# Kernel optimization log

Hardware: AMD Instinct MI355X
Metric: run time of the kernel (lower is better)

## Reference

```python
import jax, jax.numpy as jnp
import numpy as np

B, N, D, H = 2, 4096, 256, 8
HD = D // H
NEG_SLOPE = 0.01
LN_EPS = 1e-5


def setup_inputs() -> dict:
    key = jax.random.key(0)
    ks = jax.random.split(key, 6)
    s = 1.0 / np.sqrt(D)
    return {
        "h": jax.random.normal(ks[0], (B, N, D), dtype=jnp.float32),
        "W_l": jax.random.normal(ks[1], (D, D), dtype=jnp.float32) * s,
        "W_r": jax.random.normal(ks[2], (D, D), dtype=jnp.float32) * s,
        "a_l": jax.random.normal(ks[3], (HD,), dtype=jnp.float32) * s,
        "a_r": jax.random.normal(ks[4], (HD,), dtype=jnp.float32) * s,
        "W_final": jax.random.normal(ks[5], (D, D), dtype=jnp.float32) * s,
        "ln_g": jnp.ones((D,), dtype=jnp.float32),
        "ln_b": jnp.zeros((D,), dtype=jnp.float32),
    }


def _leaky(x):
    return jnp.where(x >= 0, x, NEG_SLOPE * x)


def reference(h, W_l, W_r, a_l, a_r, W_final, ln_g, ln_b):
    b, n, d = h.shape
    # projections -> [b, H, n, HD]
    fl = (h @ W_l).reshape(b, n, H, HD).transpose(0, 2, 1, 3)
    fr = (h @ W_r).reshape(b, n, H, HD).transpose(0, 2, 1, 3)
    # additive GAT-style scores: [b, H, n] each, broadcast to [b, H, n, n]
    sl = jnp.einsum("bhnd,d->bhn", _leaky(fl), a_l)
    sr = jnp.einsum("bhnd,d->bhn", _leaky(fr), a_r)
    score = sl[..., :, None] + sr[..., None, :]  # [b, H, n, n]
    attn = jnp.mean(score, axis=1)  # pre-softmax mean over heads: [b, n, n]
    p = jax.nn.softmax(score, axis=-1)  # dropout is identity (eval / p=0)
    context = jnp.einsum("bhij,bhjd->bhid", p, fr)  # [b, H, n, HD]
    h_sa = context.transpose(0, 2, 1, 3).reshape(b, n, d)
    fh = h_sa @ W_final
    x = h + fh
    mu = jnp.mean(x, axis=-1, keepdims=True)
    var = jnp.mean(jnp.square(x - mu), axis=-1, keepdims=True)
    h_out = (x - mu) * jax.lax.rsqrt(var + LN_EPS) * ln_g + ln_b
    return (h_out, attn)
```

## Files before the change

kernel.cpp:

```cpp
#include <hip/hip_runtime.h>
#include <hip/hip_bf16.h>

#define BATCH 2
#define SEQ   4096
#define DIM   256
#define HEADS 8
#define HDIM  32
#define M_ROWS (BATCH * SEQ)
#define JCHUNK 32
#define NCHUNK (SEQ / JCHUNK)

typedef short bf16x8 __attribute__((ext_vector_type(8)));
typedef unsigned short u16x8 __attribute__((ext_vector_type(8)));
typedef float f32x4 __attribute__((ext_vector_type(4)));

static __device__ inline unsigned short f2bf(float x) {
  union { float f; unsigned u; } v; v.f = x;
  unsigned r = v.u + 0x7FFF + ((v.u >> 16) & 1);
  return (unsigned short)(r >> 16);
}

__global__ __launch_bounds__(256) void k_prep(const float* __restrict__ Wl,
                                              const float* __restrict__ Wr,
                                              unsigned short* __restrict__ Wt) {
  __shared__ float tile[32][33];
  const int k0 = blockIdx.x * 32;
  const int n0 = blockIdx.y * 32;
  const int t = threadIdx.x;
  const float* W = (n0 < 256) ? Wl : Wr;
  const int nb = n0 & 255;
  {
    const int r = t >> 3;
    const int c = (t & 7) * 4;
    const float4 v = *(const float4*)(&W[(size_t)(k0 + r) * DIM + nb + c]);
    tile[r][c + 0] = v.x; tile[r][c + 1] = v.y;
    tile[r][c + 2] = v.z; tile[r][c + 3] = v.w;
  }
  __syncthreads();
  {
    const int nl = t >> 3;
    const int kl = (t & 7) * 4;
    ushort4 o;
    o.x = f2bf(tile[kl + 0][nl]); o.y = f2bf(tile[kl + 1][nl]);
    o.z = f2bf(tile[kl + 2][nl]); o.w = f2bf(tile[kl + 3][nl]);
    *(ushort4*)(&Wt[(size_t)(n0 + nl) * DIM + k0 + kl]) = o;
  }
}

__global__ __launch_bounds__(512) void k_gemm_fused(
    const float* __restrict__ A, const unsigned short* __restrict__ Wt,
    const float* __restrict__ a_l, const float* __restrict__ a_r,
    float* __restrict__ fr, float* __restrict__ sr,
    float* __restrict__ msl, float* __restrict__ msr) {
  __shared__ unsigned short As[64 * 32];
  __shared__ unsigned short Bs[256 * 32];
  __shared__ float red[64][8];

  const int bid = blockIdx.x;
  const int isR = bid & 1;
  const int bm  = bid >> 1;
  const int m0 = bm * 64;
  const int n0 = isR * 256;

  const int t = threadIdx.x;
  const int lane = t & 63;
  const int wid = t >> 6;

  f32x4 acc[4][2];
  #pragma unroll
  for (int i = 0; i < 4; ++i)
    #pragma unroll
    for (int j = 0; j < 2; ++j) acc[i][j] = (f32x4){0.f, 0.f, 0.f, 0.f};

  for (int k0 = 0; k0 < DIM; k0 += 32) {
    if (t < 256) {
      const int row = t >> 2;
      const int kc = t & 3;
      const int slot = kc ^ ((row >> 1) & 3);
      const float4 a0 = *(const float4*)(&A[(size_t)(m0 + row) * DIM + k0 + kc * 8]);
      const float4 a1 = *(const float4*)(&A[(size_t)(m0 + row) * DIM + k0 + kc * 8 + 4]);
      u16x8 pa;
      pa[0] = f2bf(a0.x); pa[1] = f2bf(a0.y); pa[2] = f2bf(a0.z); pa[3] = f2bf(a0.w);
      pa[4] = f2bf(a1.x); pa[5] = f2bf(a1.y); pa[6] = f2bf(a1.z); pa[7] = f2bf(a1.w);
      *(u16x8*)((char*)As + row * 64 + slot * 16) = pa;
    }
    #pragma unroll
    for (int p = 0; p < 2; ++p) {
      const int task = t + p * 512;
      const int row = task >> 2;
      const int kc = task & 3;
      const int slot = kc ^ ((row >> 1) & 3);
      const u16x8 pb = *(const u16x8*)(&Wt[(size_t)(n0 + row) * DIM + k0 + kc * 8]);
      *(u16x8*)((char*)Bs + row * 64 + slot * 16) = pb;
    }
    __syncthreads();

    bf16x8 af[4], bfr[2];
    #pragma unroll
    for (int mr = 0; mr < 4; ++mr) {
      const int ra = mr * 16 + (lane & 15);
      const int sl = (lane >> 4) ^ ((ra >> 1) & 3);
      af[mr] = *(const bf16x8*)((const char*)As + ra * 64 + sl * 16);
    }
    #pragma unroll
    for (int nr = 0; nr < 2; ++nr) {
      const int cb = wid * 32 + nr * 16 + (lane & 15);
      const int sl = (lane >> 4) ^ ((cb >> 1) & 3);
      bfr[nr] = *(const bf16x8*)((const char*)Bs + cb * 64 + sl * 16);
    }
    #pragma unroll
    for (int mr = 0; mr < 4; ++mr)
      #pragma unroll
      for (int nr = 0; nr < 2; ++nr)
        acc[mr][nr] = __builtin_amdgcn_mfma_f32_16x16x32_bf16(af[mr], bfr[nr], acc[mr][nr], 0, 0, 0);
    __syncthreads();
  }

  const float* av = isR ? a_r : a_l;
  const int b = m0 >> 12;
  const int nbase = m0 & 4095;

  #pragma unroll
  for (int mr = 0; mr < 4; ++mr) {
    #pragma unroll
    for (int r = 0; r < 4; ++r) {
      float p = 0.f;
      #pragma unroll
      for (int nr = 0; nr < 2; ++nr) {
        float x = acc[mr][nr][r];
        x = x >= 0.f ? x : 0.01f * x;
        p = fmaf(x, av[nr * 16 + (lane & 15)], p);
      }
      #pragma unroll
      for (int o = 1; o < 16; o <<= 1) p += __shfl_xor(p, o, 16);
      if ((lane & 15) == 0) {
        const int rl = mr * 16 + (lane >> 4) * 4 + r;
        red[rl][wid] = p;
        if (isR) sr[((size_t)(b * HEADS + wid)) * SEQ + nbase + rl] = p;
      }
    }
  }
  __syncthreads();
  if (t < 64) {
    float s = 0.f;
    #pragma unroll
    for (int h2 = 0; h2 < 8; ++h2) s += red[t][h2];
    (isR ? msr : msl)[m0 + t] = s * 0.125f;
  }
  if (isR) {
    #pragma unroll
    for (int mr = 0; mr < 4; ++mr)
      #pragma unroll
      for (int nr = 0; nr < 2; ++nr) {
        const int col = wid * 32 + nr * 16 + (lane & 15);
        #pragma unroll
        for (int r = 0; r < 4; ++r) {
          const int row = m0 + mr * 16 + (lane >> 4) * 4 + r;
          fr[(size_t)row * DIM + col] = acc[mr][nr][r];
        }
      }
  }
}

__global__ __launch_bounds__(256) void k_ctx(const float* __restrict__ sr,
                                             const float* __restrict__ fr,
                                             float* __restrict__ cpart,
                                             float* __restrict__ wpart) {
  const int b  = blockIdx.x >> 7;
  const int jc = blockIdx.x & 127;
  const int j0 = jc * JCHUNK;
  const int t = threadIdx.x;
  __shared__ float ws_[HEADS][JCHUNK];

  {
    const int h2 = t >> 5, jj = t & 31;
    float e = expf(sr[((size_t)(b * HEADS + h2)) * SEQ + j0 + jj]);
    ws_[h2][jj] = e;
    float s = e;
    #pragma unroll
    for (int o = 16; o > 0; o >>= 1) s += __shfl_xor(s, o, 32);
    if (jj == 0) wpart[(size_t)(b * NCHUNK + jc) * HEADS + h2] = s;
  }
  __syncthreads();

  const int h2 = t >> 5;
  const float* frb = fr + (size_t)(b * SEQ + j0) * DIM + t;
  float accv = 0.f;
  #pragma unroll 8
  for (int jj = 0; jj < JCHUNK; ++jj)
    accv = fmaf(ws_[h2][jj], frb[(size_t)jj * DIM], accv);
  cpart[(size_t)(b * NCHUNK + jc) * DIM + t] = accv;
}

__global__ __launch_bounds__(256) void k_fh(const float* __restrict__ cpart,
                                            const float* __restrict__ wpart,
                                            const float* __restrict__ Wf,
                                            float* __restrict__ fhp) {
  const int b = blockIdx.x >> 3;
  const int kc = blockIdx.x & 7;
  const int t = threadIdx.x;
  __shared__ float credu[8][32];
  __shared__ float c_s[32];
  __shared__ float wred[128];

  {
    const int jg = t >> 5, kl = t & 31;
    float p = 0.f;
    #pragma unroll
    for (int jc = jg; jc < NCHUNK; jc += 8)
      p += cpart[(size_t)(b * NCHUNK + jc) * DIM + kc * HDIM + kl];
    credu[jg][kl] = p;
  }
  if (t < 128) wred[t] = wpart[(size_t)(b * NCHUNK + t) * HEADS + kc];
  __syncthreads();
  if (t < 32) {
    float s = 0.f;
    #pragma unroll
    for (int g2 = 0; g2 < 8; ++g2) s += credu[g2][t];
    float wsum = 0.f;
    #pragma unroll
    for (int i = 0; i < 128; ++i) wsum += wred[i];
    c_s[t] = s / wsum;
  }
  __syncthreads();

  float a2 = 0.f;
  #pragma unroll 8
  for (int kl = 0; kl < HDIM; ++kl)
    a2 = fmaf(c_s[kl], Wf[(size_t)(kc * HDIM + kl) * DIM + t], a2);
  fhp[(size_t)(b * HEADS + kc) * DIM + t] = a2;
}

__global__ __launch_bounds__(256) void k_ln_attn(const float* __restrict__ h,
                                                 const float* __restrict__ fhp,
                                                 const float* __restrict__ g,
                                                 const float* __restrict__ bb,
                                                 const float* __restrict__ msl,
                                                 const float* __restrict__ msr,
                                                 float* __restrict__ out,
                                                 float* __restrict__ attn) {
  const int row = blockIdx.x;
  const int b = row >> 12;
  const int t = threadIdx.x;
  float fh = 0.f;
  #pragma unroll
  for (int h2 = 0; h2 < 8; ++h2) fh += fhp[(size_t)(b * HEADS + h2) * DIM + t];
  const float x = h[(size_t)row * DIM + t] + fh;
  float s1 = x, s2 = x * x;
  #pragma unroll
  for (int o = 32; o > 0; o >>= 1) {
    s1 += __shfl_xor(s1, o, 64);
    s2 += __shfl_xor(s2, o, 64);
  }
  __shared__ float r1[4], r2[4];
  if ((t & 63) == 0) { r1[t >> 6] = s1; r2[t >> 6] = s2; }
  __syncthreads();
  s1 = r1[0] + r1[1] + r1[2] + r1[3];
  s2 = r2[0] + r2[1] + r2[2] + r2[3];
  const float mu = s1 * (1.f / 256.f);
  const float var = s2 * (1.f / 256.f) - mu * mu;
  const float rs = rsqrtf(var + 1e-5f);
  out[(size_t)row * DIM + t] = (x - mu) * rs * g[t] + bb[t];

  const float v = msl[row];
  const f32x4* mr4 = (const f32x4*)(msr + ((size_t)b << 12));
  f32x4* dst = (f32x4*)(attn + ((size_t)row << 12));
  #pragma unroll
  for (int q = 0; q < 4; ++q) {
    f32x4 m4 = mr4[q * 256 + t];
    __builtin_nontemporal_store(m4 + v, &dst[q * 256 + t]);
  }
}

extern "C" void kernel_launch(void* const* d_in, const int* in_sizes, int n_in,
                              void* d_out, int out_size, void* d_ws, size_t ws_size,
                              hipStream_t stream) {
  const float* h  = (const float*)d_in[0];
  const float* Wl = (const float*)d_in[1];
  const float* Wr = (const float*)d_in[2];
  const float* al = (const float*)d_in[3];
  const float* ar = (const float*)d_in[4];
  const float* Wf = (const float*)d_in[5];
  const float* g  = (const float*)d_in[6];
  const float* bb = (const float*)d_in[7];
  float* out = (float*)d_out;
  float* ws  = (float*)d_ws;

  float* fr    = ws;
  float* srs   = fr + (size_t)M_ROWS * DIM;
  float* msl   = srs + BATCH * HEADS * SEQ;
  float* msr   = msl + M_ROWS;
  float* cpart = msr + M_ROWS;
  float* wpart = cpart + BATCH * NCHUNK * DIM;
  float* fhp   = wpart + BATCH * NCHUNK * HEADS;
  unsigned short* Wt = (unsigned short*)(fhp + BATCH * HEADS * DIM);

  k_prep<<<dim3(8, 16), 256, 0, stream>>>(Wl, Wr, Wt);
  k_gemm_fused<<<256, 512, 0, stream>>>(h, Wt, al, ar, fr, srs, msl, msr);
  k_ctx<<<BATCH * NCHUNK, 256, 0, stream>>>(srs, fr, cpart, wpart);
  k_fh<<<BATCH * HEADS, 256, 0, stream>>>(cpart, wpart, Wf, fhp);
  k_ln_attn<<<M_ROWS, 256, 0, stream>>>(h, fhp, g, bb, msl, msr,
                                        out, out + (size_t)M_ROWS * DIM);
}
```

Measured before the change: 56.97 us.

## Merge ctx, fh and attn-store into one kernel with last-block reduction

Combines the context partial kernel, the Wf projection kernel and the large attn broadcast store into one launch. The ctx blocks take a global atomic counter, and the last one to finish reduces the partials and computes fh for both batches. The remaining blocks write the attn matrix at the same time. LayerNorm becomes its own small kernel that reads the finished fh. The aim is to remove launch gaps and to overlap the serial ctx→fh chain with the bandwidth-heavy attn writes. The cost is that a single block does the whole Wf GEMV serially, and correctness now depends on the counter being reset in k_prep on every call.

```diff
diff --git a/kernel.cpp b/kernel.cpp
--- a/kernel.cpp
+++ b/kernel.cpp
@@ -9,6 +9,7 @@
 #define M_ROWS (BATCH * SEQ)
 #define JCHUNK 32
 #define NCHUNK (SEQ / JCHUNK)
+#define CTXBLKS (BATCH * NCHUNK)
 
 typedef short bf16x8 __attribute__((ext_vector_type(8)));
 typedef unsigned short u16x8 __attribute__((ext_vector_type(8)));
@@ -22,7 +23,9 @@
 
 __global__ __launch_bounds__(256) void k_prep(const float* __restrict__ Wl,
                                               const float* __restrict__ Wr,
-                                              unsigned short* __restrict__ Wt) {
+                                              unsigned short* __restrict__ Wt,
+                                              unsigned* __restrict__ ctr) {
+  if (blockIdx.x == 0 && blockIdx.y == 0 && threadIdx.x == 0) *ctr = 0u;
   __shared__ float tile[32][33];
   const int k0 = blockIdx.x * 32;
   const int n0 = blockIdx.y * 32;
@@ -162,90 +165,95 @@
   }
 }
 
-__global__ __launch_bounds__(256) void k_ctx(const float* __restrict__ sr,
-                                             const float* __restrict__ fr,
-                                             float* __restrict__ cpart,
-                                             float* __restrict__ wpart) {
-  const int b  = blockIdx.x >> 7;
-  const int jc = blockIdx.x & 127;
-  const int j0 = jc * JCHUNK;
+__global__ __launch_bounds__(256) void k_mega(const float* __restrict__ sr,
+                                              const float* __restrict__ fr,
+                                              const float* __restrict__ Wf,
+                                              const float* __restrict__ msl,
+                                              const float* __restrict__ msr,
+                                              float* __restrict__ cpart,
+                                              float* __restrict__ wpart,
+                                              float* __restrict__ fh2,
+                                              float* __restrict__ attn,
+                                              unsigned* __restrict__ ctr) {
+  const int blk = blockIdx.x;
   const int t = threadIdx.x;
   __shared__ float ws_[HEADS][JCHUNK];
-
-  {
-    const int h2 = t >> 5, jj = t & 31;
-    float e = expf(sr[((size_t)(b * HEADS + h2)) * SEQ + j0 + jj]);
-    ws_[h2][jj] = e;
-    float s = e;
-    #pragma unroll
-    for (int o = 16; o > 0; o >>= 1) s += __shfl_xor(s, o, 32);
-    if (jj == 0) wpart[(size_t)(b * NCHUNK + jc) * HEADS + h2] = s;
-  }
-  __syncthreads();
-
-  const int h2 = t >> 5;
-  const float* frb = fr + (size_t)(b * SEQ + j0) * DIM + t;
-  float accv = 0.f;
-  #pragma unroll 8
-  for (int jj = 0; jj < JCHUNK; ++jj)
-    accv = fmaf(ws_[h2][jj], frb[(size_t)jj * DIM], accv);
-  cpart[(size_t)(b * NCHUNK + jc) * DIM + t] = accv;
-}
-
-__global__ __launch_bounds__(256) void k_fh(const float* __restrict__ cpart,
-                                            const float* __restrict__ wpart,
-                                            const float* __restrict__ Wf,
-                                            float* __restrict__ fhp) {
-  const int b = blockIdx.x >> 3;
-  const int kc = blockIdx.x & 7;
-  const int t = threadIdx.x;
-  __shared__ float credu[8][32];
-  __shared__ float c_s[32];
-  __shared__ float wred[128];
-
-  {
-    const int jg = t >> 5, kl = t & 31;
-    float p = 0.f;
-    #pragma unroll
-    for (int jc = jg; jc < NCHUNK; jc += 8)
-      p += cpart[(size_t)(b * NCHUNK + jc) * DIM + kc * HDIM + kl];
-    credu[jg][kl] = p;
-  }
-  if (t < 128) wred[t] = wpart[(size_t)(b * NCHUNK + t) * HEADS + kc];
-  __syncthreads();
-  if (t < 32) {
-    float s = 0.f;
-    #pragma unroll
-    for (int g2 = 0; g2 < 8; ++g2) s += credu[g2][t];
-    float wsum = 0.f;
-    #pragma unroll
-    for (int i = 0; i < 128; ++i) wsum += wred[i];
-    c_s[t] = s / wsum;
-  }
-  __syncthreads();
-
-  float a2 = 0.f;
-  #pragma unroll 8
-  for (int kl = 0; kl < HDIM; ++kl)
-    a2 = fmaf(c_s[kl], Wf[(size_t)(kc * HDIM + kl) * DIM + t], a2);
-  fhp[(size_t)(b * HEADS + kc) * DIM + t] = a2;
-}
-
-__global__ __launch_bounds__(256) void k_ln_attn(const float* __restrict__ h,
-                                                 const float* __restrict__ fhp,
-                                                 const float* __restrict__ g,
-                                                 const float* __restrict__ bb,
-                                                 const float* __restrict__ msl,
-                                                 const float* __restrict__ msr,
-                                                 float* __restrict__ out,
-                                                 float* __restrict__ attn) {
+  __shared__ float wred[HEADS];
+  __shared__ float c_s[DIM];
+  __shared__ unsigned done_s;
+
+  if (blk < CTXBLKS) {
+    const int b  = blk >> 7;
+    const int jc = blk & 127;
+    const int j0 = jc * JCHUNK;
+    {
+      const int h2 = t >> 5, jj = t & 31;
+      float e = expf(sr[((size_t)(b * HEADS + h2)) * SEQ + j0 + jj]);
+      ws_[h2][jj] = e;
+      float s = e;
+      #pragma unroll
+      for (int o = 16; o > 0; o >>= 1) s += __shfl_xor(s, o, 32);
+      if (jj == 0) wpart[(size_t)(b * NCHUNK + jc) * HEADS + h2] = s;
+    }
+    __syncthreads();
+    {
+      const int h2 = t >> 5;
+      const float* frb = fr + (size_t)(b * SEQ + j0) * DIM + t;
+      float accv = 0.f;
+      #pragma unroll 8
+      for (int jj = 0; jj < JCHUNK; ++jj)
+        accv = fmaf(ws_[h2][jj], frb[(size_t)jj * DIM], accv);
+      cpart[(size_t)(b * NCHUNK + jc) * DIM + t] = accv;
+    }
+    __threadfence();
+    if (t == 0) done_s = atomicAdd(ctr, 1u);
+    __syncthreads();
+    if (done_s == CTXBLKS - 1) {
+      __threadfence();
+      for (int b2 = 0; b2 < BATCH; ++b2) {
+        if (t < HEADS) {
+          float s = 0.f;
+          for (int jc2 = 0; jc2 < NCHUNK; ++jc2)
+            s += wpart[(size_t)(b2 * NCHUNK + jc2) * HEADS + t];
+          wred[t] = s;
+        }
+        float c = 0.f;
+        for (int jc2 = 0; jc2 < NCHUNK; ++jc2)
+          c += cpart[(size_t)(b2 * NCHUNK + jc2) * DIM + t];
+        __syncthreads();
+        c_s[t] = c / wred[t >> 5];
+        __syncthreads();
+        float a2 = 0.f;
+        #pragma unroll 8
+        for (int k = 0; k < DIM; ++k)
+          a2 = fmaf(c_s[k], Wf[(size_t)k * DIM + t], a2);
+        fh2[b2 * DIM + t] = a2;
+        __syncthreads();
+      }
+    }
+  } else {
+    const int row = blk - CTXBLKS;
+    const int b = row >> 12;
+    const float v = msl[row];
+    const f32x4* mr4 = (const f32x4*)(msr + ((size_t)b << 12));
+    f32x4* dst = (f32x4*)(attn + ((size_t)row << 12));
+    #pragma unroll
+    for (int q = 0; q < 4; ++q) {
+      f32x4 m4 = mr4[q * 256 + t];
+      __builtin_nontemporal_store(m4 + v, &dst[q * 256 + t]);
+    }
+  }
+}
+
+__global__ __launch_bounds__(256) void k_ln(const float* __restrict__ h,
+                                            const float* __restrict__ fh2,
+                                            const float* __restrict__ g,
+                                            const float* __restrict__ bb,
+                                            float* __restrict__ out) {
   const int row = blockIdx.x;
   const int b = row >> 12;
   const int t = threadIdx.x;
-  float fh = 0.f;
-  #pragma unroll
-  for (int h2 = 0; h2 < 8; ++h2) fh += fhp[(size_t)(b * HEADS + h2) * DIM + t];
-  const float x = h[(size_t)row * DIM + t] + fh;
+  const float x = h[(size_t)row * DIM + t] + fh2[b * DIM + t];
   float s1 = x, s2 = x * x;
   #pragma unroll
   for (int o = 32; o > 0; o >>= 1) {
@@ -261,15 +269,6 @@
   const float var = s2 * (1.f / 256.f) - mu * mu;
   const float rs = rsqrtf(var + 1e-5f);
   out[(size_t)row * DIM + t] = (x - mu) * rs * g[t] + bb[t];
-
-  const float v = msl[row];
-  const f32x4* mr4 = (const f32x4*)(msr + ((size_t)b << 12));
-  f32x4* dst = (f32x4*)(attn + ((size_t)row << 12));
-  #pragma unroll
-  for (int q = 0; q < 4; ++q) {
-    f32x4 m4 = mr4[q * 256 + t];
-    __builtin_nontemporal_store(m4 + v, &dst[q * 256 + t]);
-  }
 }
 
 extern "C" void kernel_launch(void* const* d_in, const int* in_sizes, int n_in,
@@ -292,13 +291,14 @@
   float* msr   = msl + M_ROWS;
   float* cpart = msr + M_ROWS;
   float* wpart = cpart + BATCH * NCHUNK * DIM;
-  float* fhp   = wpart + BATCH * NCHUNK * HEADS;
-  unsigned short* Wt = (unsigned short*)(fhp + BATCH * HEADS * DIM);
-
-  k_prep<<<dim3(8, 16), 256, 0, stream>>>(Wl, Wr, Wt);
+  float* fh2   = wpart + BATCH * NCHUNK * HEADS;
+  unsigned short* Wt = (unsigned short*)(fh2 + BATCH * DIM);
+  unsigned* ctr = (unsigned*)(Wt + 512 * DIM);
+
+  k_prep<<<dim3(8, 16), 256, 0, stream>>>(Wl, Wr, Wt, ctr);
   k_gemm_fused<<<256, 512, 0, stream>>>(h, Wt, al, ar, fr, srs, msl, msr);
-  k_ctx<<<BATCH * NCHUNK, 256, 0, stream>>>(srs, fr, cpart, wpart);
-  k_fh<<<BATCH * HEADS, 256, 0, stream>>>(cpart, wpart, Wf, fhp);
-  k_ln_attn<<<M_ROWS, 256, 0, stream>>>(h, fhp, g, bb, msl, msr,
-                                        out, out + (size_t)M_ROWS * DIM);
-}
+  k_mega<<<CTXBLKS + M_ROWS, 256, 0, stream>>>(srs, fr, Wf, msl, msr,
+                                               cpart, wpart, fh2,
+                                               out + (size_t)M_ROWS * DIM, ctr);
+  k_ln<<<M_ROWS, 256, 0, stream>>>(h, fh2, g, bb, out);
+}
```

Result: slower. 105.3 us (+84.8%).
